# Kernel tuning notes

Hardware: AMD Instinct MI355X
Metric: run time of the kernel (lower is better)

## Reference

```python
import jax, jax.numpy as jnp
import numpy as np

B, NQ, NK, D, H = 4, 1024, 1024, 1024, 16
HD = D // H
SCALE = HD ** -0.5
LN_EPS = 1e-5


def setup_inputs() -> dict:
    key = jax.random.key(0)
    ks = jax.random.split(key, 16)
    s = 0.02
    inp = {
        "query": jax.random.normal(ks[0], (B, NQ, D), jnp.float32),
        "key": jax.random.normal(ks[1], (B, NK, D), jnp.float32),
        "value": jax.random.normal(ks[2], (B, NK, D), jnp.float32),
        # attention projections (torch Linear: [out, in] weights)
        "wq": jax.random.normal(ks[3], (D, D), jnp.float32) * s,
        "bq": jnp.zeros((D,), jnp.float32),
        "wk": jax.random.normal(ks[4], (D, D), jnp.float32) * s,
        "bk": jnp.zeros((D,), jnp.float32),
        "wv": jax.random.normal(ks[5], (D, D), jnp.float32) * s,
        "bv": jnp.zeros((D,), jnp.float32),
        "wo": jax.random.normal(ks[6], (D, D), jnp.float32) * s,
        "bo": jnp.zeros((D,), jnp.float32),
        # vad_proj: Linear(D, D//2) -> GELU -> Linear(D//2, 3) -> Tanh
        "w1": jax.random.normal(ks[7], (D // 2, D), jnp.float32) * s,
        "b1": jnp.zeros((D // 2,), jnp.float32),
        "w2": jax.random.normal(ks[8], (3, D // 2), jnp.float32) * s,
        "b2": jnp.zeros((3,), jnp.float32),
        "vad_lambda": jnp.asarray(0.1, jnp.float32),
        "ln_g": jnp.ones((D,), jnp.float32),
        "ln_b": jnp.zeros((D,), jnp.float32),
    }
    return inp


def _vad(x, w1, b1, w2, b2):
    h = jax.nn.gelu(x @ w1.T + b1, approximate=False)
    return jnp.tanh(h @ w2.T + b2)  # [B, N, 3]


def _layer_norm(x, g, b):
    mu = jnp.mean(x, axis=-1, keepdims=True)
    var = jnp.mean(jnp.square(x - mu), axis=-1, keepdims=True)
    return (x - mu) * jax.lax.rsqrt(var + LN_EPS) * g + b


def reference(query, key, value, wq, bq, wk, bk, wv, bv, wo, bo,
              w1, b1, w2, b2, vad_lambda, ln_g, ln_b):
    Bq, Nq, Dm = query.shape
    Nk = key.shape[1]
    # project and split heads: [B, H, N, HD]
    Q = (query @ wq.T + bq).reshape(Bq, Nq, H, HD).transpose(0, 2, 1, 3)
    K = (key @ wk.T + bk).reshape(Bq, Nk, H, HD).transpose(0, 2, 1, 3)
    V = (value @ wv.T + bv).reshape(Bq, Nk, H, HD).transpose(0, 2, 1, 3)
    scores = jnp.einsum("bhqd,bhkd->bhqk", Q, K) * SCALE  # [B,H,Nq,Nk]
    # VAD affinity: -||v_q[i] - v_k[j]||_2
    vq = _vad(query, w1, b1, w2, b2)  # [B,Nq,3]
    vk = _vad(key, w1, b1, w2, b2)    # [B,Nk,3]
    diff = vq[:, :, None, :] - vk[:, None, :, :]         # [B,Nq,Nk,3]
    affinity = -jnp.sqrt(jnp.sum(diff * diff, axis=-1))  # [B,Nq,Nk]
    guided = scores + vad_lambda * affinity[:, None, :, :]
    attn = jax.nn.softmax(guided, axis=-1)
    out = jnp.einsum("bhqk,bhkd->bhqd", attn, V)
    out = out.transpose(0, 2, 1, 3).reshape(Bq, Nq, Dm)
    out = out @ wo.T + bo
    return _layer_norm(query + out, ln_g, ln_b)
```

## Files before the change

kernel.cpp:

```cpp
#include <hip/hip_runtime.h>
#include <hip/hip_bf16.h>

typedef float f32x4 __attribute__((ext_vector_type(4)));
typedef float f32x16 __attribute__((ext_vector_type(16)));
typedef __bf16 bf16x8 __attribute__((ext_vector_type(8)));
typedef unsigned short us8 __attribute__((ext_vector_type(8)));
typedef unsigned short us4 __attribute__((ext_vector_type(4)));

#define DEVI __device__ __forceinline__
#define LOG2E 1.44269504088896f

DEVI unsigned short f2bf(float x) {
  return __builtin_bit_cast(unsigned short, __float2bfloat16(x));
}
DEVI float bf2f(unsigned short u) {
  return __builtin_bit_cast(float, ((unsigned int)u) << 16);
}
DEVI bf16x8 ldb8(const unsigned short* p) {
  return __builtin_bit_cast(bf16x8, *(const us8*)p);
}
DEVI void gload16(const unsigned short* g, unsigned short* l) {
  __builtin_amdgcn_global_load_lds(
      (const __attribute__((address_space(1))) unsigned int*)(const void*)g,
      (__attribute__((address_space(3))) unsigned int*)(void*)l, 16, 0, 0);
}

__global__ __launch_bounds__(256) void cvt_all(const float* __restrict__ q, const float* __restrict__ k,
                                               const float* __restrict__ v,
                                               const float* __restrict__ wq, const float* __restrict__ wk,
                                               const float* __restrict__ wv, const float* __restrict__ wo,
                                               const float* __restrict__ w1,
                                               unsigned short* __restrict__ qb, unsigned short* __restrict__ kb,
                                               unsigned short* __restrict__ vb,
                                               unsigned short* __restrict__ wqb, unsigned short* __restrict__ wkb,
                                               unsigned short* __restrict__ wvb, unsigned short* __restrict__ wob,
                                               unsigned short* __restrict__ w1b) {
  const int bx = blockIdx.x;
  const float* in;
  unsigned short* out;
  int i;
  if (bx < 6144) {
    int which = bx >> 11;
    in = which == 0 ? q : which == 1 ? k : v;
    out = which == 0 ? qb : which == 1 ? kb : vb;
    i = ((bx & 2047) * 256 + threadIdx.x) * 8;
  } else if (bx < 8192) {
    int which = (bx - 6144) >> 9;
    in = which == 0 ? wq : which == 1 ? wk : which == 2 ? wv : wo;
    out = which == 0 ? wqb : which == 1 ? wkb : which == 2 ? wvb : wob;
    i = (((bx - 6144) & 511) * 256 + threadIdx.x) * 8;
  } else {
    in = w1;
    out = w1b;
    i = ((bx - 8192) * 256 + threadIdx.x) * 8;
  }
  float4 a = *(const float4*)(in + i);
  float4 b = *(const float4*)(in + i + 4);
  us8 r = {f2bf(a.x), f2bf(a.y), f2bf(a.z), f2bf(a.w), f2bf(b.x), f2bf(b.y), f2bf(b.z), f2bf(b.w)};
  *(us8*)(out + i) = r;
}

template <int EPI>
DEVI void gemm_body(const unsigned short* __restrict__ A, const unsigned short* __restrict__ W,
                    const float* __restrict__ bias, void* __restrict__ Cout,
                    int N, int K, int lda, float oscale, int brow, int bcol,
                    unsigned short* As, unsigned short* Bs, int t) {
  const int l = t & 63;
  const int w4 = t >> 6, wr = w4 >> 1, wc = w4 & 1;
  const int l5 = l & 31, hi = l >> 5;
  f32x16 acc[2][2] = {};
  for (int kt = 0; kt < K; kt += 64) {
    __syncthreads();
#pragma unroll
    for (int i = 0; i < 4; ++i) {
      int c = t + i * 256;
      int row = c >> 3;
      int sw = (((c & 7) ^ (row & 7) ^ ((row >> 3) & 3))) * 8;
      gload16(A + (size_t)(brow + row) * lda + kt + sw, As + c * 8);
      gload16(W + (size_t)(bcol + row) * lda + kt + sw, Bs + c * 8);
    }
    __syncthreads();
#pragma unroll
    for (int ks = 0; ks < 4; ++ks) {
      bf16x8 af[2], bfr[2];
      const int ch = (ks * 2 + hi) ^ (l5 & 7) ^ ((l5 >> 3) & 3);
#pragma unroll
      for (int mi = 0; mi < 2; ++mi)
        af[mi] = ldb8(&As[(wr * 64 + mi * 32 + l5) * 64 + ch * 8]);
#pragma unroll
      for (int ni = 0; ni < 2; ++ni)
        bfr[ni] = ldb8(&Bs[(wc * 64 + ni * 32 + l5) * 64 + ch * 8]);
#pragma unroll
      for (int mi = 0; mi < 2; ++mi)
#pragma unroll
        for (int ni = 0; ni < 2; ++ni)
          acc[mi][ni] = __builtin_amdgcn_mfma_f32_32x32x16_bf16(af[mi], bfr[ni], acc[mi][ni], 0, 0, 0);
    }
  }
#pragma unroll
  for (int mi = 0; mi < 2; ++mi)
#pragma unroll
    for (int ni = 0; ni < 2; ++ni) {
      int col = bcol + wc * 64 + ni * 32 + l5;
      int rowBase = brow + wr * 64 + mi * 32 + hi * 4;
      float bc = (EPI == 3) ? 0.f : bias[col];
#pragma unroll
      for (int reg = 0; reg < 16; ++reg) {
        int row = rowBase + (reg & 3) + 8 * (reg >> 2);
        float v;
        if (EPI == 3)
          v = (acc[mi][ni][reg] + bias[row]) * oscale;
        else if (EPI == 2)
          v = acc[mi][ni][reg] + 0.5f * bc;
        else
          v = (acc[mi][ni][reg] + bc) * oscale;
        if (EPI == 1) v = 0.5f * v * (1.0f + erff(v * 0.70710678118f));
        ((unsigned short*)Cout)[(size_t)row * N + col] = f2bf(v);
      }
    }
}

__global__ __launch_bounds__(256) void proj_k(const unsigned short* __restrict__ qb, const unsigned short* __restrict__ kb,
                                              const unsigned short* __restrict__ vb,
                                              const unsigned short* __restrict__ wqb, const unsigned short* __restrict__ wkb,
                                              const unsigned short* __restrict__ wvb, const unsigned short* __restrict__ w1b,
                                              const float* __restrict__ bq, const float* __restrict__ bk,
                                              const float* __restrict__ bv, const float* __restrict__ b1,
                                              unsigned short* __restrict__ Qp, unsigned short* __restrict__ Kp,
                                              unsigned short* __restrict__ Vt,
                                              unsigned short* __restrict__ h1q, unsigned short* __restrict__ h1k) {
  __shared__ unsigned short As[8192];
  __shared__ unsigned short Bs[8192];
  const int t = threadIdx.x;
  const int lin = blockIdx.x;
  const int nl = (lin & 7) * 128 + (lin >> 3);
  if (nl < 256) {
    gemm_body<0>(qb, wqb, bq, Qp, 1024, 1024, 1024, 0.125f * LOG2E,
                 (nl >> 3) * 128, (nl & 7) * 128, As, Bs, t);
  } else if (nl < 512) {
    int s = nl - 256;
    gemm_body<0>(kb, wkb, bk, Kp, 1024, 1024, 1024, 1.f,
                 (s >> 3) * 128, (s & 7) * 128, As, Bs, t);
  } else if (nl < 768) {
    int s = nl - 512;
    gemm_body<3>(wvb, vb, bv, Vt, 4096, 1024, 1024, 1.f,
                 (s >> 5) * 128, (s & 31) * 128, As, Bs, t);
  } else {
    int s = nl - 768;
    const unsigned short* A = (s >= 128) ? kb : qb;
    unsigned short* C = (s >= 128) ? h1k : h1q;
    int s2 = s & 127;
    gemm_body<1>(A, w1b, b1, C, 512, 1024, 1024, 1.f,
                 (s2 >> 2) * 128, (s2 & 3) * 128, As, Bs, t);
  }
}

__global__ __launch_bounds__(256) void wo_k(const unsigned short* __restrict__ Obuf, const unsigned short* __restrict__ wob,
                                            const float* __restrict__ bo,
                                            unsigned short* __restrict__ tmpA, unsigned short* __restrict__ tmpB) {
  __shared__ unsigned short As[8192];
  __shared__ unsigned short Bs[8192];
  const int t = threadIdx.x;
  const int lin = blockIdx.x;
  const int nl = (lin & 7) * 64 + (lin >> 3);
  const int z = nl >> 8, s = nl & 255;
  gemm_body<2>(Obuf + z * 512, wob + z * 512, bo, z ? tmpB : tmpA,
               1024, 512, 1024, 1.f, (s >> 3) * 128, (s & 7) * 128, As, Bs, t);
}

__global__ __launch_bounds__(256) void vad2_k(const unsigned short* __restrict__ h1a, const unsigned short* __restrict__ h1b,
                                              const float* __restrict__ w2, const float* __restrict__ b2,
                                              float* __restrict__ outa, float* __restrict__ outb) {
  const unsigned short* h1 = blockIdx.y ? h1b : h1a;
  float* out = blockIdx.y ? outb : outa;
  const int t = threadIdx.x, l = t & 63, w = t >> 6;
  const int row = blockIdx.x * 4 + w;
  us8 hv = *(const us8*)(h1 + (size_t)row * 512 + l * 8);
  float hf[8];
#pragma unroll
  for (int j = 0; j < 8; ++j) hf[j] = bf2f(hv[j]);
  float s[3];
#pragma unroll
  for (int c = 0; c < 3; ++c) {
    const float* wp = w2 + c * 512 + l * 8;
    float a = 0.f;
#pragma unroll
    for (int j = 0; j < 8; ++j) a += hf[j] * wp[j];
    s[c] = a;
  }
#pragma unroll
  for (int m = 1; m < 64; m <<= 1) {
#pragma unroll
    for (int c = 0; c < 3; ++c) s[c] += __shfl_xor(s[c], m, 64);
  }
  if (l == 0) {
#pragma unroll
    for (int c = 0; c < 3; ++c) out[(size_t)row * 3 + c] = tanhf(s[c] + b2[c]);
  }
}

__global__ __launch_bounds__(256) void aff_k(const float* __restrict__ vq, const float* __restrict__ vk,
                                             const float* __restrict__ plam, unsigned short* __restrict__ aff) {
  __shared__ float vqs[64][3], vks[64][3];
  const int t = threadIdx.x;
  const int b = blockIdx.z, q0 = blockIdx.y * 64, k0 = blockIdx.x * 64;
  const float lam2 = plam[0] * LOG2E;
  if (t < 192) {
    ((float*)vqs)[t] = vq[((size_t)b * 1024 + q0) * 3 + t];
    ((float*)vks)[t] = vk[((size_t)b * 1024 + k0) * 3 + t];
  }
  __syncthreads();
  const int q = t >> 2, kc = (t & 3) * 16;
  const float a0 = vqs[q][0], a1 = vqs[q][1], a2 = vqs[q][2];
  unsigned short o[16];
#pragma unroll
  for (int j = 0; j < 16; ++j) {
    int k = kc + j;
    float dx = a0 - vks[k][0], dy = a1 - vks[k][1], dz = a2 - vks[k][2];
    o[j] = f2bf(-lam2 * sqrtf(dx * dx + dy * dy + dz * dz));
  }
  unsigned short* dst = aff + ((size_t)(b * 1024 + q0 + q)) * 1024 + k0 + kc;
  *(us8*)dst = *(us8*)&o[0];
  *(us8*)(dst + 8) = *(us8*)&o[8];
}

__global__ __launch_bounds__(512, 6) void attn_k(const unsigned short* __restrict__ Qp,
                                                 const unsigned short* __restrict__ Kp,
                                                 const unsigned short* __restrict__ Vt,
                                                 const unsigned short* __restrict__ aff,
                                                 unsigned short* __restrict__ Obuf) {
  __shared__ unsigned short Ks[2][4096];
  __shared__ unsigned short Vs[2][4096];
  __shared__ unsigned short Ps[8][1024];
  const int lin = blockIdx.x + 8 * (blockIdx.y + 16 * blockIdx.z);
  const int nl = (lin & 7) * 64 + (lin >> 3);
  const int qb = nl & 7, h = (nl >> 3) & 15, b = nl >> 7;
  const int t = threadIdx.x, l = t & 63, w = t >> 6;
  const int l4 = l & 15, lg = l >> 4;
  const size_t qrow0 = (size_t)b * 1024 + qb * 128;
  const int hoff = h * 64;

  bf16x8 qf[2];
#pragma unroll
  for (int ks = 0; ks < 2; ++ks)
    qf[ks] = ldb8(Qp + (qrow0 + w * 16 + l4) * 1024 + hoff + ks * 32 + lg * 8);

  {
    const unsigned short* gk = Kp + ((size_t)b * 1024) * 1024 + hoff;
    const unsigned short* gv = Vt + (size_t)hoff * 4096 + (size_t)b * 1024;
    int c = t, row = c >> 3, sw = ((c & 7) ^ (row & 7)) * 8;
    gload16(gk + (size_t)row * 1024 + sw, Ks[0] + c * 8);
    gload16(gv + (size_t)row * 4096 + sw, Vs[0] + c * 8);
  }
  float l_run = 0.f;
  f32x4 accO[4] = {};
  const unsigned short* ab = aff + (qrow0 + w * 16 + l4) * 1024 + lg * 4;
  __syncthreads();

  int cur = 0;
  for (int kt = 0; kt < 16; ++kt) {
    if (kt < 15) {
      const unsigned short* gk = Kp + ((size_t)b * 1024 + (kt + 1) * 64) * 1024 + hoff;
      const unsigned short* gv = Vt + (size_t)hoff * 4096 + (size_t)b * 1024 + (kt + 1) * 64;
      int c = t, row = c >> 3, sw = ((c & 7) ^ (row & 7)) * 8;
      gload16(gk + (size_t)row * 1024 + sw, Ks[cur ^ 1] + c * 8);
      gload16(gv + (size_t)row * 4096 + sw, Vs[cur ^ 1] + c * 8);
    }
    f32x4 sc[4];
#pragma unroll
    for (int jt = 0; jt < 4; ++jt) {
      us4 av = *(const us4*)(ab + kt * 64 + jt * 16);
#pragma unroll
      for (int r = 0; r < 4; ++r) sc[jt][r] = bf2f(av[r]);
    }
    __builtin_amdgcn_s_setprio(1);
#pragma unroll
    for (int jt = 0; jt < 4; ++jt) {
#pragma unroll
      for (int ks = 0; ks < 2; ++ks) {
        bf16x8 kf = ldb8(&Ks[cur][(jt * 16 + l4) * 64 + (((ks * 4 + lg) ^ (l4 & 7))) * 8]);
        sc[jt] = __builtin_amdgcn_mfma_f32_16x16x32_bf16(kf, qf[ks], sc[jt], 0, 0, 0);
      }
    }
    __builtin_amdgcn_s_setprio(0);
    float pv[4][4];
    float rs = 0.f;
#pragma unroll
    for (int jt = 0; jt < 4; ++jt)
#pragma unroll
      for (int r = 0; r < 4; ++r) { pv[jt][r] = exp2f(sc[jt][r]); rs += pv[jt][r]; }
    l_run += rs;
    char* pw = (char*)&Ps[w][0];
#pragma unroll
    for (int jt = 0; jt < 4; ++jt) {
      unsigned int p0, p1;
      asm("v_cvt_pk_bf16_f32 %0, %1, %2" : "=v"(p0) : "v"(pv[jt][0]), "v"(pv[jt][1]));
      asm("v_cvt_pk_bf16_f32 %0, %1, %2" : "=v"(p1) : "v"(pv[jt][2]), "v"(pv[jt][3]));
      int chunk = (jt * 2 + (lg >> 1)) ^ (l4 & 7);
      *(unsigned long long*)(pw + l4 * 128 + chunk * 16 + (lg & 1) * 8) =
          (unsigned long long)p0 | ((unsigned long long)p1 << 32);
    }
    __builtin_amdgcn_s_setprio(1);
#pragma unroll
    for (int js = 0; js < 2; ++js) {
      bf16x8 pa = ldb8(&Ps[w][l4 * 64 + (((js * 4 + lg) ^ (l4 & 7))) * 8]);
#pragma unroll
      for (int dt = 0; dt < 4; ++dt) {
        bf16x8 vf = ldb8(&Vs[cur][(dt * 16 + l4) * 64 + (((js * 4 + lg) ^ (l4 & 7))) * 8]);
        accO[dt] = __builtin_amdgcn_mfma_f32_16x16x32_bf16(pa, vf, accO[dt], 0, 0, 0);
      }
    }
    __builtin_amdgcn_s_setprio(0);
    __syncthreads();
    cur ^= 1;
  }
  l_run += __shfl_xor(l_run, 16, 64);
  l_run += __shfl_xor(l_run, 32, 64);
  float linv = 1.f / l_run;
  float lr[4];
#pragma unroll
  for (int r = 0; r < 4; ++r) lr[r] = __shfl(linv, lg * 4 + r, 16);
#pragma unroll
  for (int dt = 0; dt < 4; ++dt)
#pragma unroll
    for (int r = 0; r < 4; ++r) {
      float v = accO[dt][r] * lr[r];
      Obuf[(qrow0 + w * 16 + lg * 4 + r) * 1024 + hoff + dt * 16 + l4] = f2bf(v);
    }
}

__global__ __launch_bounds__(256) void ln_k(const float* __restrict__ q,
                                            const unsigned short* __restrict__ ta,
                                            const unsigned short* __restrict__ tb,
                                            const float* __restrict__ g,
                                            const float* __restrict__ bb,
                                            float* __restrict__ out) {
  __shared__ float red[8];
  const int row = blockIdx.x, t = threadIdx.x;
  const int l = t & 63, w = t >> 6;
  const size_t base = (size_t)row * 1024 + t * 4;
  float4 a = *(const float4*)(q + base);
  us4 cv = *(const us4*)(ta + base);
  us4 dv = *(const us4*)(tb + base);
  float x0 = a.x + bf2f(cv[0]) + bf2f(dv[0]);
  float x1 = a.y + bf2f(cv[1]) + bf2f(dv[1]);
  float x2 = a.z + bf2f(cv[2]) + bf2f(dv[2]);
  float x3 = a.w + bf2f(cv[3]) + bf2f(dv[3]);
  float s = x0 + x1 + x2 + x3;
#pragma unroll
  for (int m = 1; m < 64; m <<= 1) s += __shfl_xor(s, m, 64);
  if (l == 0) red[w] = s;
  __syncthreads();
  float mean = (red[0] + red[1] + red[2] + red[3]) * (1.f / 1024.f);
  float d0 = x0 - mean, d1 = x1 - mean, d2 = x2 - mean, d3 = x3 - mean;
  float v = d0 * d0 + d1 * d1 + d2 * d2 + d3 * d3;
#pragma unroll
  for (int m = 1; m < 64; m <<= 1) v += __shfl_xor(v, m, 64);
  if (l == 0) red[4 + w] = v;
  __syncthreads();
  float var = (red[4] + red[5] + red[6] + red[7]) * (1.f / 1024.f);
  float rstd = rsqrtf(var + 1e-5f);
  float4 gv = *(const float4*)(g + t * 4);
  float4 bv = *(const float4*)(bb + t * 4);
  float4 o;
  o.x = d0 * rstd * gv.x + bv.x;
  o.y = d1 * rstd * gv.y + bv.y;
  o.z = d2 * rstd * gv.z + bv.z;
  o.w = d3 * rstd * gv.w + bv.w;
  *(float4*)(out + (size_t)row * 1024 + t * 4) = o;
}

extern "C" void kernel_launch(void* const* d_in, const int* in_sizes, int n_in,
                              void* d_out, int out_size, void* d_ws, size_t ws_size,
                              hipStream_t stream) {
  const float* query = (const float*)d_in[0];
  const float* key_  = (const float*)d_in[1];
  const float* value = (const float*)d_in[2];
  const float* wq = (const float*)d_in[3];
  const float* bq = (const float*)d_in[4];
  const float* wk = (const float*)d_in[5];
  const float* bk = (const float*)d_in[6];
  const float* wv = (const float*)d_in[7];
  const float* bv = (const float*)d_in[8];
  const float* wo = (const float*)d_in[9];
  const float* bo = (const float*)d_in[10];
  const float* w1 = (const float*)d_in[11];
  const float* b1 = (const float*)d_in[12];
  const float* w2 = (const float*)d_in[13];
  const float* b2 = (const float*)d_in[14];
  const float* lam = (const float*)d_in[15];
  const float* lng = (const float*)d_in[16];
  const float* lnb = (const float*)d_in[17];

  char* ws = (char*)d_ws;
  size_t off = 0;
  auto alloc = [&](size_t n) { char* p = ws + off; off += (n + 255) & ~(size_t)255; return p; };
  unsigned short* qb  = (unsigned short*)alloc(8388608);
  unsigned short* kb  = (unsigned short*)alloc(8388608);
  unsigned short* vb  = (unsigned short*)alloc(8388608);
  unsigned short* wqb = (unsigned short*)alloc(2097152);
  unsigned short* wkb = (unsigned short*)alloc(2097152);
  unsigned short* wvb = (unsigned short*)alloc(2097152);
  unsigned short* wob = (unsigned short*)alloc(2097152);
  unsigned short* w1b = (unsigned short*)alloc(1048576);
  unsigned short* Qp  = (unsigned short*)alloc(8388608);
  unsigned short* Kp  = (unsigned short*)alloc(8388608);
  unsigned short* Vt  = (unsigned short*)alloc(8388608);
  unsigned short* h1q = (unsigned short*)alloc(4194304);
  unsigned short* h1k = (unsigned short*)alloc(4194304);
  float* vadq = (float*)alloc(49152);
  float* vadk = (float*)alloc(49152);
  unsigned short* Obuf = (unsigned short*)alloc(8388608);
  unsigned short* aff  = vb;
  unsigned short* tmpA = qb;
  unsigned short* tmpB = kb;

  cvt_all<<<8448, 256, 0, stream>>>(query, key_, value, wq, wk, wv, wo, w1,
                                    qb, kb, vb, wqb, wkb, wvb, wob, w1b);

  proj_k<<<1024, 256, 0, stream>>>(qb, kb, vb, wqb, wkb, wvb, w1b,
                                   bq, bk, bv, b1, Qp, Kp, Vt, h1q, h1k);
  vad2_k<<<dim3(1024, 2), 256, 0, stream>>>(h1q, h1k, w2, b2, vadq, vadk);
  aff_k<<<dim3(16, 16, 4), 256, 0, stream>>>(vadq, vadk, lam, aff);
  attn_k<<<dim3(8, 16, 4), 512, 0, stream>>>(Qp, Kp, Vt, aff, Obuf);
  wo_k<<<512, 256, 0, stream>>>(Obuf, wob, bo, tmpA, tmpB);
  ln_k<<<4096, 256, 0, stream>>>(query, tmpA, tmpB, lng, lnb, (float*)d_out);
}
```

Baseline: 153.3 us.

## Process two 16-row query groups per wave in attention kernel

The attention kernel now runs 4 waves (256 threads) per block instead of 8, and each wave handles 32 query rows as two 16-row groups. Each K and V fragment read from LDS now feeds two MFMAs, halving LDS reads per MFMA and raising per-wave instruction-level parallelism. In exchange, register pressure per wave roughly doubles for accumulators and scores, fewer waves are available per block to hide latency, and the K/V tile load loop is split across fewer threads.

```diff
diff --git a/kernel.cpp b/kernel.cpp
--- a/kernel.cpp
+++ b/kernel.cpp
@@ -224,14 +224,14 @@
   *(us8*)(dst + 8) = *(us8*)&o[8];
 }
 
-__global__ __launch_bounds__(512, 6) void attn_k(const unsigned short* __restrict__ Qp,
+__global__ __launch_bounds__(256, 3) void attn_k(const unsigned short* __restrict__ Qp,
                                                  const unsigned short* __restrict__ Kp,
                                                  const unsigned short* __restrict__ Vt,
                                                  const unsigned short* __restrict__ aff,
                                                  unsigned short* __restrict__ Obuf) {
   __shared__ unsigned short Ks[2][4096];
   __shared__ unsigned short Vs[2][4096];
-  __shared__ unsigned short Ps[8][1024];
+  __shared__ unsigned short Ps[4][2048];
   const int lin = blockIdx.x + 8 * (blockIdx.y + 16 * blockIdx.z);
   const int nl = (lin & 7) * 64 + (lin >> 3);
   const int qb = nl & 7, h = (nl >> 3) & 15, b = nl >> 7;
@@ -240,21 +240,27 @@
   const size_t qrow0 = (size_t)b * 1024 + qb * 128;
   const int hoff = h * 64;
 
-  bf16x8 qf[2];
-#pragma unroll
-  for (int ks = 0; ks < 2; ++ks)
-    qf[ks] = ldb8(Qp + (qrow0 + w * 16 + l4) * 1024 + hoff + ks * 32 + lg * 8);
+  bf16x8 qf[2][2];
+#pragma unroll
+  for (int g = 0; g < 2; ++g)
+#pragma unroll
+    for (int ks = 0; ks < 2; ++ks)
+      qf[g][ks] = ldb8(Qp + (qrow0 + w * 32 + g * 16 + l4) * 1024 + hoff + ks * 32 + lg * 8);
 
   {
     const unsigned short* gk = Kp + ((size_t)b * 1024) * 1024 + hoff;
     const unsigned short* gv = Vt + (size_t)hoff * 4096 + (size_t)b * 1024;
-    int c = t, row = c >> 3, sw = ((c & 7) ^ (row & 7)) * 8;
-    gload16(gk + (size_t)row * 1024 + sw, Ks[0] + c * 8);
-    gload16(gv + (size_t)row * 4096 + sw, Vs[0] + c * 8);
-  }
-  float l_run = 0.f;
-  f32x4 accO[4] = {};
-  const unsigned short* ab = aff + (qrow0 + w * 16 + l4) * 1024 + lg * 4;
+#pragma unroll
+    for (int i = 0; i < 2; ++i) {
+      int c = t + i * 256, row = c >> 3, sw = ((c & 7) ^ (row & 7)) * 8;
+      gload16(gk + (size_t)row * 1024 + sw, Ks[0] + c * 8);
+      gload16(gv + (size_t)row * 4096 + sw, Vs[0] + c * 8);
+    }
+  }
+  float l_run[2] = {0.f, 0.f};
+  f32x4 accO[2][4] = {};
+  const unsigned short* ab0 = aff + (qrow0 + w * 32 + l4) * 1024 + lg * 4;
+  const unsigned short* ab1 = ab0 + 16 * 1024;
   __syncthreads();
 
   int cur = 0;
@@ -262,16 +268,20 @@
     if (kt < 15) {
       const unsigned short* gk = Kp + ((size_t)b * 1024 + (kt + 1) * 64) * 1024 + hoff;
       const unsigned short* gv = Vt + (size_t)hoff * 4096 + (size_t)b * 1024 + (kt + 1) * 64;
-      int c = t, row = c >> 3, sw = ((c & 7) ^ (row & 7)) * 8;
-      gload16(gk + (size_t)row * 1024 + sw, Ks[cur ^ 1] + c * 8);
-      gload16(gv + (size_t)row * 4096 + sw, Vs[cur ^ 1] + c * 8);
-    }
-    f32x4 sc[4];
+#pragma unroll
+      for (int i = 0; i < 2; ++i) {
+        int c = t + i * 256, row = c >> 3, sw = ((c & 7) ^ (row & 7)) * 8;
+        gload16(gk + (size_t)row * 1024 + sw, Ks[cur ^ 1] + c * 8);
+        gload16(gv + (size_t)row * 4096 + sw, Vs[cur ^ 1] + c * 8);
+      }
+    }
+    f32x4 sc[2][4];
 #pragma unroll
     for (int jt = 0; jt < 4; ++jt) {
-      us4 av = *(const us4*)(ab + kt * 64 + jt * 16);
-#pragma unroll
-      for (int r = 0; r < 4; ++r) sc[jt][r] = bf2f(av[r]);
+      us4 a0 = *(const us4*)(ab0 + kt * 64 + jt * 16);
+      us4 a1 = *(const us4*)(ab1 + kt * 64 + jt * 16);
+#pragma unroll
+      for (int r = 0; r < 4; ++r) { sc[0][jt][r] = bf2f(a0[r]); sc[1][jt][r] = bf2f(a1[r]); }
     }
     __builtin_amdgcn_s_setprio(1);
 #pragma unroll
@@ -279,54 +289,63 @@
 #pragma unroll
       for (int ks = 0; ks < 2; ++ks) {
         bf16x8 kf = ldb8(&Ks[cur][(jt * 16 + l4) * 64 + (((ks * 4 + lg) ^ (l4 & 7))) * 8]);
-        sc[jt] = __builtin_amdgcn_mfma_f32_16x16x32_bf16(kf, qf[ks], sc[jt], 0, 0, 0);
+#pragma unroll
+        for (int g = 0; g < 2; ++g)
+          sc[g][jt] = __builtin_amdgcn_mfma_f32_16x16x32_bf16(kf, qf[g][ks], sc[g][jt], 0, 0, 0);
       }
     }
     __builtin_amdgcn_s_setprio(0);
-    float pv[4][4];
-    float rs = 0.f;
-#pragma unroll
-    for (int jt = 0; jt < 4; ++jt)
-#pragma unroll
-      for (int r = 0; r < 4; ++r) { pv[jt][r] = exp2f(sc[jt][r]); rs += pv[jt][r]; }
-    l_run += rs;
-    char* pw = (char*)&Ps[w][0];
-#pragma unroll
-    for (int jt = 0; jt < 4; ++jt) {
-      unsigned int p0, p1;
-      asm("v_cvt_pk_bf16_f32 %0, %1, %2" : "=v"(p0) : "v"(pv[jt][0]), "v"(pv[jt][1]));
-      asm("v_cvt_pk_bf16_f32 %0, %1, %2" : "=v"(p1) : "v"(pv[jt][2]), "v"(pv[jt][3]));
-      int chunk = (jt * 2 + (lg >> 1)) ^ (l4 & 7);
-      *(unsigned long long*)(pw + l4 * 128 + chunk * 16 + (lg & 1) * 8) =
-          (unsigned long long)p0 | ((unsigned long long)p1 << 32);
+#pragma unroll
+    for (int g = 0; g < 2; ++g) {
+      float rs = 0.f;
+      char* pw = (char*)&Ps[w][g * 1024];
+#pragma unroll
+      for (int jt = 0; jt < 4; ++jt) {
+        float p0f = exp2f(sc[g][jt][0]), p1f = exp2f(sc[g][jt][1]);
+        float p2f = exp2f(sc[g][jt][2]), p3f = exp2f(sc[g][jt][3]);
+        rs += (p0f + p1f) + (p2f + p3f);
+        unsigned int p0, p1;
+        asm("v_cvt_pk_bf16_f32 %0, %1, %2" : "=v"(p0) : "v"(p0f), "v"(p1f));
+        asm("v_cvt_pk_bf16_f32 %0, %1, %2" : "=v"(p1) : "v"(p2f), "v"(p3f));
+        int chunk = (jt * 2 + (lg >> 1)) ^ (l4 & 7);
+        *(unsigned long long*)(pw + l4 * 128 + chunk * 16 + (lg & 1) * 8) =
+            (unsigned long long)p0 | ((unsigned long long)p1 << 32);
+      }
+      l_run[g] += rs;
     }
     __builtin_amdgcn_s_setprio(1);
 #pragma unroll
     for (int js = 0; js < 2; ++js) {
-      bf16x8 pa = ldb8(&Ps[w][l4 * 64 + (((js * 4 + lg) ^ (l4 & 7))) * 8]);
+      bf16x8 pa0 = ldb8(&Ps[w][l4 * 64 + (((js * 4 + lg) ^ (l4 & 7))) * 8]);
+      bf16x8 pa1 = ldb8(&Ps[w][1024 + l4 * 64 + (((js * 4 + lg) ^ (l4 & 7))) * 8]);
 #pragma unroll
       for (int dt = 0; dt < 4; ++dt) {
         bf16x8 vf = ldb8(&Vs[cur][(dt * 16 + l4) * 64 + (((js * 4 + lg) ^ (l4 & 7))) * 8]);
-        accO[dt] = __builtin_amdgcn_mfma_f32_16x16x32_bf16(pa, vf, accO[dt], 0, 0, 0);
+        accO[0][dt] = __builtin_amdgcn_mfma_f32_16x16x32_bf16(pa0, vf, accO[0][dt], 0, 0, 0);
+        accO[1][dt] = __builtin_amdgcn_mfma_f32_16x16x32_bf16(pa1, vf, accO[1][dt], 0, 0, 0);
       }
     }
     __builtin_amdgcn_s_setprio(0);
     __syncthreads();
     cur ^= 1;
   }
-  l_run += __shfl_xor(l_run, 16, 64);
-  l_run += __shfl_xor(l_run, 32, 64);
-  float linv = 1.f / l_run;
-  float lr[4];
-#pragma unroll
-  for (int r = 0; r < 4; ++r) lr[r] = __shfl(linv, lg * 4 + r, 16);
-#pragma unroll
-  for (int dt = 0; dt < 4; ++dt)
-#pragma unroll
-    for (int r = 0; r < 4; ++r) {
-      float v = accO[dt][r] * lr[r];
-      Obuf[(qrow0 + w * 16 + lg * 4 + r) * 1024 + hoff + dt * 16 + l4] = f2bf(v);
-    }
+#pragma unroll
+  for (int g = 0; g < 2; ++g) {
+    float lr_ = l_run[g];
+    lr_ += __shfl_xor(lr_, 16, 64);
+    lr_ += __shfl_xor(lr_, 32, 64);
+    float linv = 1.f / lr_;
+    float lr[4];
+#pragma unroll
+    for (int r = 0; r < 4; ++r) lr[r] = __shfl(linv, lg * 4 + r, 16);
+#pragma unroll
+    for (int dt = 0; dt < 4; ++dt)
+#pragma unroll
+      for (int r = 0; r < 4; ++r) {
+        float v = accO[g][dt][r] * lr[r];
+        Obuf[(qrow0 + w * 32 + g * 16 + lg * 4 + r) * 1024 + hoff + dt * 16 + l4] = f2bf(v);
+      }
+  }
 }
 
 __global__ __launch_bounds__(256) void ln_k(const float* __restrict__ q,
@@ -422,7 +441,7 @@
                                    bq, bk, bv, b1, Qp, Kp, Vt, h1q, h1k);
   vad2_k<<<dim3(1024, 2), 256, 0, stream>>>(h1q, h1k, w2, b2, vadq, vadk);
   aff_k<<<dim3(16, 16, 4), 256, 0, stream>>>(vadq, vadk, lam, aff);
-  attn_k<<<dim3(8, 16, 4), 512, 0, stream>>>(Qp, Kp, Vt, aff, Obuf);
+  attn_k<<<dim3(8, 16, 4), 256, 0, stream>>>(Qp, Kp, Vt, aff, Obuf);
   wo_k<<<512, 256, 0, stream>>>(Obuf, wob, bo, tmpA, tmpB);
   ln_k<<<4096, 256, 0, stream>>>(query, tmpA, tmpB, lng, lnb, (float*)d_out);
 }
```

New measurement: 157.4 us. +2.7%, slower.
